# Kernel optimization log

Hardware: AMD Instinct MI355X
Metric: run time of the kernel (lower is better)

The kernel has to match this reference:

```python
import itertools
import jax, jax.numpy as jnp
import numpy as np

BATCH = 32
GRID = (128, 128)        # self.shape
X_COLS = 64              # x embeds into every other column (di=2)
NUM_LAYERS = 4
KERNEL = (2, 2)          # center offset = (k-1)//2 = 0 -> window taps {0,1} per dim
NINPUTS = 4              # prod(KERNEL)
NCOMBOS = 16             # 2**NINPUTS


def setup_inputs() -> dict:
    key = jax.random.key(0)
    k1, k2 = jax.random.split(key)
    x = jax.random.uniform(k1, (BATCH, GRID[0], X_COLS), dtype=jnp.float32)
    toggle_gates = jax.random.normal(k2, (NUM_LAYERS, NCOMBOS) + GRID, dtype=jnp.float32)
    return {"x": x, "toggle_gates": toggle_gates}


def _bitmask():
    # rows m: bits (b0..b3), b0 most significant -- matches itertools.product order
    return jnp.asarray(np.array(list(itertools.product(range(2), repeat=NINPUTS)),
                                dtype=np.float32))  # (16, 4)


def reference(x, toggle_gates):
    # x: (B, 128, 64), toggle_gates: (L, 16, 128, 128)
    B = x.shape[0]
    d1, d2 = GRID
    bitmask = _bitmask()                         # (16, 4)
    tw = jax.nn.sigmoid(toggle_gates)            # (L, 16, d1, d2)

    # embed: even columns of the grid hold x, odd columns are scratch memory (zeros)
    state = jnp.zeros((B, d1, d2), dtype=x.dtype).at[:, :, ::2].set(x)

    k1, k2 = KERNEL
    for layer in range(NUM_LAYERS):
        # convolve: periodic sliding window, taps at offsets {0..k-1} (center=0)
        # feature index = i1*k2 + i2 (row-major), value = state[(p1+i1)%d1, (p2+i2)%d2]
        conv = jnp.stack(
            [jnp.roll(jnp.roll(state, -i1, axis=1), -i2, axis=2)
             for i1 in range(k1) for i2 in range(k2)],
            axis=-1)                             # (B, d1, d2, 4)
        # soft bitmask match: weight[m] = prod_j (1 - |bit(m,j) - conv_j|)
        w = jnp.prod(1.0 - jnp.abs(bitmask[:, None, None, None, :] - conv[None]),
                     axis=-1)                    # (16, B, d1, d2)
        state = jnp.clip(jnp.einsum('mbxy,mxy->bxy', w, tw[layer]), 0.0, 1.0)

    # unembed: read back the input wire positions
    return state[:, :, ::2]
```

## Files before the change

kernel.cpp:

```cpp
#include <hip/hip_runtime.h>

#define D1 128
#define D2 128
#define XC 64
#define NBH 16
#define RS 16
#define RR 12
#define BSTR (RR * RS)
#define B1 (NBH * BSTR)
#define NTH 192
#define PLANE 16384

__device__ __forceinline__ float fast_sigmoid(float v) {
    return __builtin_amdgcn_rcpf(1.0f + __expf(-v));
}
__device__ __forceinline__ float clamp01(float r) {
    return fminf(fmaxf(r, 0.0f), 1.0f);
}

__device__ __forceinline__ void compute_layer(float* __restrict__ st, int src, int dst,
                                              int sbase, const float g[16]) {
    float d[8];
#pragma unroll
    for (int k = 0; k < 8; ++k) d[k] = g[2 * k + 1] - g[2 * k];
#pragma unroll
    for (int b = 0; b < NBH; ++b) {
        const float* sb = st + src + b * BSTR + sbase;
        const float f0 = sb[0], f1 = sb[1], f2 = sb[RS], f3 = sb[RS + 1];
        float u[8];
#pragma unroll
        for (int k = 0; k < 8; ++k) u[k] = fmaf(f3, d[k], g[2 * k]);
        float v[4];
#pragma unroll
        for (int k = 0; k < 4; ++k) v[k] = fmaf(f2, u[2 * k + 1] - u[2 * k], u[2 * k]);
        float w[2];
#pragma unroll
        for (int k = 0; k < 2; ++k) w[k] = fmaf(f1, v[2 * k + 1] - v[2 * k], v[2 * k]);
        st[dst + b * BSTR + sbase] = clamp01(fmaf(f0, w[1] - w[0], w[0]));
    }
}

__global__ __launch_bounds__(NTH) void fused_kernel(const float* __restrict__ x,
                                                    const float* __restrict__ tg,
                                                    float* __restrict__ out) {
    __shared__ float st[2 * B1 + 64];

    const int tid  = threadIdx.x;
    const int tile = blockIdx.x & 255;
    const int b0   = (blockIdx.x >> 8) * NBH;

    const int q1 = tid >> 4;
    const int q2 = tid & 15;
    const bool act = (q2 < RR);

    const int t1 = ((tile >> 4) & 15) << 3;
    const int t2 = (tile & 15) << 3;
    const int p1 = (t1 + q1) & (D1 - 1);
    const int p2 = (t2 + q2) & (D2 - 1);
    const int sbase = (q1 << 4) | q2;
    const int modd = p2 & 1;
    const float* gcell = tg + (p1 << 7) + p2;

    if (act) {
        if (!modd) {
            const float* xp = x + ((size_t)b0 * D1 + p1) * XC + (p2 >> 1);
#pragma unroll
            for (int b = 0; b < NBH; ++b)
                st[b * BSTR + sbase] = xp[(size_t)b * (D1 * XC)];
        } else {
#pragma unroll
            for (int b = 0; b < NBH; ++b)
                st[b * BSTR + sbase] = 0.0f;
        }
    }

    float g0[4];
    float graw[16];
    if (act) {
#pragma unroll
        for (int j = 0; j < 4; ++j) {
            const int m = modd ? ((j >> 1) * 4 + (j & 1)) : ((j >> 1) * 8 + (j & 1) * 2);
            g0[j] = gcell[(size_t)m * PLANE];
        }
#pragma unroll
        for (int j = 0; j < 4; ++j) g0[j] = fast_sigmoid(g0[j]);
#pragma unroll
        for (int m = 0; m < 16; ++m) graw[m] = gcell[(size_t)(16 + m) * PLANE];
    }
    __syncthreads();

    if (act) {
        const float d10 = g0[1] - g0[0], d32 = g0[3] - g0[2];
#pragma unroll
        for (int b = 0; b < NBH; ++b) {
            const float* sb = st + b * BSTR + sbase;
            const float f0 = sb[0], f1 = sb[1], f2 = sb[RS], f3 = sb[RS + 1];
            const float fin  = modd ? f3 : f2;
            const float fout = modd ? f1 : f0;
            const float a = fmaf(fin, d10, g0[0]);
            const float c = fmaf(fin, d32, g0[2]);
            st[B1 + b * BSTR + sbase] = clamp01(fmaf(fout, c - a, a));
        }
    }
    __syncthreads();

    float g[16];
    if (act) {
#pragma unroll
        for (int m = 0; m < 16; ++m) g[m] = fast_sigmoid(graw[m]);
#pragma unroll
        for (int m = 0; m < 16; ++m) graw[m] = gcell[(size_t)(32 + m) * PLANE];
        compute_layer(st, B1, 0, sbase, g);
    }
    __syncthreads();

    const bool fact = act && (q1 < 8) && (q2 < 8) && !(q2 & 1);
    if (act) {
#pragma unroll
        for (int m = 0; m < 16; ++m) g[m] = fast_sigmoid(graw[m]);
        if (fact) {
#pragma unroll
            for (int m = 0; m < 16; ++m) graw[m] = gcell[(size_t)(48 + m) * PLANE];
        }
        compute_layer(st, 0, B1, sbase, g);
    }
    __syncthreads();

    if (fact) {
#pragma unroll
        for (int m = 0; m < 16; ++m) g[m] = fast_sigmoid(graw[m]);
        float d[8];
#pragma unroll
        for (int k = 0; k < 8; ++k) d[k] = g[2 * k + 1] - g[2 * k];
        float* op = out + ((size_t)b0 * D1 + p1) * XC + (p2 >> 1);
#pragma unroll
        for (int b = 0; b < NBH; ++b) {
            const float* sb = st + B1 + b * BSTR + sbase;
            const float f0 = sb[0], f1 = sb[1], f2 = sb[RS], f3 = sb[RS + 1];
            float u[8];
#pragma unroll
            for (int k = 0; k < 8; ++k) u[k] = fmaf(f3, d[k], g[2 * k]);
            float v[4];
#pragma unroll
            for (int k = 0; k < 4; ++k) v[k] = fmaf(f2, u[2 * k + 1] - u[2 * k], u[2 * k]);
            float w[2];
#pragma unroll
            for (int k = 0; k < 2; ++k) w[k] = fmaf(f1, v[2 * k + 1] - v[2 * k], v[2 * k]);
            op[(size_t)b * (D1 * XC)] = clamp01(fmaf(f0, w[1] - w[0], w[0]));
        }
    }
}

extern "C" void kernel_launch(void* const* d_in, const int* in_sizes, int n_in,
                              void* d_out, int out_size, void* d_ws, size_t ws_size,
                              hipStream_t stream) {
    const float* x  = (const float*)d_in[0];
    const float* tg = (const float*)d_in[1];
    float* out = (float*)d_out;

    fused_kernel<<<512, NTH, 0, stream>>>(x, tg, out);
}
```

Baseline: 15.39 us.

## Read x directly for first layer and spread final layer across more threads

The first layer now reads its two needed inputs straight from global x instead of staging the embedded grid in shared memory. This removes one shared-memory write pass and one barrier. Gate prefetches are reordered so the next layer's loads are issued before the current sigmoid and compute. The last layer is remapped so 128 threads each handle 4 batches, replacing 32 threads each handling 16, which spreads the final compute and stores. The cost is more global loads from x in the first layer and extra gate loads in a different pattern for the last layer.

```diff
diff --git a/kernel.cpp b/kernel.cpp
--- a/kernel.cpp
+++ b/kernel.cpp
@@ -55,27 +55,15 @@
 
     const int t1 = ((tile >> 4) & 15) << 3;
     const int t2 = (tile & 15) << 3;
-    const int p1 = (t1 + q1) & (D1 - 1);
-    const int p2 = (t2 + q2) & (D2 - 1);
+    const int p1  = (t1 + q1) & (D1 - 1);
+    const int p2  = (t2 + q2) & (D2 - 1);
+    const int p1n = (p1 + 1) & (D1 - 1);
+    const int p2n = (p2 + 1) & (D2 - 1);
     const int sbase = (q1 << 4) | q2;
     const int modd = p2 & 1;
     const float* gcell = tg + (p1 << 7) + p2;
 
-    if (act) {
-        if (!modd) {
-            const float* xp = x + ((size_t)b0 * D1 + p1) * XC + (p2 >> 1);
-#pragma unroll
-            for (int b = 0; b < NBH; ++b)
-                st[b * BSTR + sbase] = xp[(size_t)b * (D1 * XC)];
-        } else {
-#pragma unroll
-            for (int b = 0; b < NBH; ++b)
-                st[b * BSTR + sbase] = 0.0f;
-        }
-    }
-
-    float g0[4];
-    float graw[16];
+    float g0[4], graw[16];
     if (act) {
 #pragma unroll
         for (int j = 0; j < 4; ++j) {
@@ -83,59 +71,67 @@
             g0[j] = gcell[(size_t)m * PLANE];
         }
 #pragma unroll
-        for (int j = 0; j < 4; ++j) g0[j] = fast_sigmoid(g0[j]);
-#pragma unroll
         for (int m = 0; m < 16; ++m) graw[m] = gcell[(size_t)(16 + m) * PLANE];
     }
-    __syncthreads();
 
     if (act) {
+#pragma unroll
+        for (int j = 0; j < 4; ++j) g0[j] = fast_sigmoid(g0[j]);
         const float d10 = g0[1] - g0[0], d32 = g0[3] - g0[2];
+        const int c = (modd ? p2n : p2) >> 1;
+        const float* xo = x + ((size_t)b0 * D1 + p1)  * XC + c;
+        const float* xi = x + ((size_t)b0 * D1 + p1n) * XC + c;
 #pragma unroll
         for (int b = 0; b < NBH; ++b) {
-            const float* sb = st + b * BSTR + sbase;
-            const float f0 = sb[0], f1 = sb[1], f2 = sb[RS], f3 = sb[RS + 1];
-            const float fin  = modd ? f3 : f2;
-            const float fout = modd ? f1 : f0;
-            const float a = fmaf(fin, d10, g0[0]);
-            const float c = fmaf(fin, d32, g0[2]);
-            st[B1 + b * BSTR + sbase] = clamp01(fmaf(fout, c - a, a));
+            const float fout = xo[(size_t)b * (D1 * XC)];
+            const float fin  = xi[(size_t)b * (D1 * XC)];
+            const float a_ = fmaf(fin, d10, g0[0]);
+            const float c_ = fmaf(fin, d32, g0[2]);
+            st[B1 + b * BSTR + sbase] = clamp01(fmaf(fout, c_ - a_, a_));
         }
     }
     __syncthreads();
 
-    float g[16];
+    float g[16], graw2[16];
     if (act) {
 #pragma unroll
+        for (int m = 0; m < 16; ++m) graw2[m] = gcell[(size_t)(32 + m) * PLANE];
+#pragma unroll
         for (int m = 0; m < 16; ++m) g[m] = fast_sigmoid(graw[m]);
-#pragma unroll
-        for (int m = 0; m < 16; ++m) graw[m] = gcell[(size_t)(32 + m) * PLANE];
         compute_layer(st, B1, 0, sbase, g);
     }
     __syncthreads();
 
-    const bool fact = act && (q1 < 8) && (q2 < 8) && !(q2 & 1);
+    const int c1 = (tid >> 2) & 7;
+    const int c2 = tid & 3;
+    const int bh = tid >> 5;
+    const int p1c = t1 + c1;
+    const int p2c = t2 + (c2 << 1);
+    const float* gcell3 = tg + (size_t)48 * PLANE + (p1c << 7) + p2c;
+
+    float graw3[16];
+    if (tid < 128) {
+#pragma unroll
+        for (int m = 0; m < 16; ++m) graw3[m] = gcell3[(size_t)m * PLANE];
+    }
     if (act) {
 #pragma unroll
-        for (int m = 0; m < 16; ++m) g[m] = fast_sigmoid(graw[m]);
-        if (fact) {
-#pragma unroll
-            for (int m = 0; m < 16; ++m) graw[m] = gcell[(size_t)(48 + m) * PLANE];
-        }
+        for (int m = 0; m < 16; ++m) g[m] = fast_sigmoid(graw2[m]);
         compute_layer(st, 0, B1, sbase, g);
     }
     __syncthreads();
 
-    if (fact) {
+    if (tid < 128) {
 #pragma unroll
-        for (int m = 0; m < 16; ++m) g[m] = fast_sigmoid(graw[m]);
+        for (int m = 0; m < 16; ++m) g[m] = fast_sigmoid(graw3[m]);
         float d[8];
 #pragma unroll
         for (int k = 0; k < 8; ++k) d[k] = g[2 * k + 1] - g[2 * k];
-        float* op = out + ((size_t)b0 * D1 + p1) * XC + (p2 >> 1);
+        const int sb3 = (c1 << 4) | (c2 << 1);
+        float* op = out + ((size_t)(b0 + bh * 4) * D1 + p1c) * XC + (p2c >> 1);
 #pragma unroll
-        for (int b = 0; b < NBH; ++b) {
-            const float* sb = st + B1 + b * BSTR + sbase;
+        for (int b = 0; b < 4; ++b) {
+            const float* sb = st + B1 + (bh * 4 + b) * BSTR + sb3;
             const float f0 = sb[0], f1 = sb[1], f2 = sb[RS], f3 = sb[RS + 1];
             float u[8];
 #pragma unroll
```

After: 14.09 us. 1.09x faster.
